# Kernel optimization log

Measured on AMD Instinct MI355X. Metric: run time of the kernel, lower is better.

## Reference

```python
import jax, jax.numpy as jnp
import numpy as np

H = 512     # LSTM_HIDDEN_SIZE
IN = 64     # LSTM_INPUT_SIZE
B = 256
T = 512
OUT = 96    # output_size (decode horizon)


def setup_inputs() -> dict:
    key = jax.random.key(0)
    ks = jax.random.split(key, 32)
    k = 1.0 / np.sqrt(H)
    u = lambda kk, shape: jax.random.uniform(kk, shape, jnp.float32, -k, k)
    inp = {"inputs": jax.random.normal(ks[0], (B, T, IN), jnp.float32)}
    shapes = {
        "enc_Wih0": (4 * H, IN), "enc_Whh0": (4 * H, H), "enc_bih0": (4 * H,), "enc_bhh0": (4 * H,),
        "enc_Wih1": (4 * H, H),  "enc_Whh1": (4 * H, H), "enc_bih1": (4 * H,), "enc_bhh1": (4 * H,),
        "dec_Wih0": (4 * H, 1),  "dec_Whh0": (4 * H, H), "dec_bih0": (4 * H,), "dec_bhh0": (4 * H,),
        "dec_Wih1": (4 * H, H),  "dec_Whh1": (4 * H, H), "dec_bih1": (4 * H,), "dec_bhh1": (4 * H,),
        "proj_W": (1, H), "proj_b": (1,),
    }
    for i, (name, sh) in enumerate(shapes.items()):
        inp[name] = u(ks[i + 1], sh)
    inp["output_size"] = OUT
    return inp


def lstm_cell(x, h, c, Wih, Whh, bih, bhh):
    # PyTorch gate order: i, f, g, o
    z = x @ Wih.T + h @ Whh.T + (bih + bhh)
    i, f, g, o = jnp.split(z, 4, axis=-1)
    c_new = jax.nn.sigmoid(f) * c + jax.nn.sigmoid(i) * jnp.tanh(g)
    h_new = jax.nn.sigmoid(o) * jnp.tanh(c_new)
    return h_new, c_new


def reference(inputs,
              enc_Wih0, enc_Whh0, enc_bih0, enc_bhh0,
              enc_Wih1, enc_Whh1, enc_bih1, enc_bhh1,
              dec_Wih0, dec_Whh0, dec_bih0, dec_bhh0,
              dec_Wih1, dec_Whh1, dec_bih1, dec_bhh1,
              proj_W, proj_b, output_size):
    bsz = inputs.shape[0]
    hdim = enc_Whh0.shape[1]
    z = jnp.zeros((bsz, hdim), inputs.dtype)

    # ---- encoder: 2-layer LSTM over time (batch_first -> time-major scan) ----
    def enc_step(carry, x_t):
        h0, c0, h1, c1 = carry
        h0, c0 = lstm_cell(x_t, h0, c0, enc_Wih0, enc_Whh0, enc_bih0, enc_bhh0)
        h1, c1 = lstm_cell(h0, h1, c1, enc_Wih1, enc_Whh1, enc_bih1, enc_bhh1)
        return (h0, c0, h1, c1), None

    xs = jnp.swapaxes(inputs, 0, 1)  # [T, B, IN]
    (h0, c0, h1, c1), _ = jax.lax.scan(enc_step, (z, z, z, z), xs)

    def dec_step(carry, _):
        h0, c0, h1, c1, x = carry  # x: [B, 1]
        h0, c0 = lstm_cell(x, h0, c0, dec_Wih0, dec_Whh0, dec_bih0, dec_bhh0)
        h1, c1 = lstm_cell(h0, h1, c1, dec_Wih1, dec_Whh1, dec_bih1, dec_bhh1)
        y = h1 @ proj_W.T + proj_b  # [B, 1]
        return (h0, c0, h1, c1, y), y

    x0 = jnp.zeros((bsz, 1), inputs.dtype)
    _, ys = jax.lax.scan(dec_step, (h0, c0, h1, c1, x0), None, length=output_size)
    # ys: [OUT, B, 1] -> [B, OUT, 1]
    return jnp.swapaxes(ys, 0, 1)
```

## Files before the change

### kernel.cpp

```cpp
#include <hip/hip_runtime.h>
#include <math.h>

#define Bb   256
#define Tt   512
#define INn  64
#define Hh   512
#define OUTn 96
#define NWG  256
#define TPB  512
#define SP   (Hh*Bb)
#define RSTRIDE 36
#define HDR  8192

struct Params {
  const float *Xt;
  float *H0, *H1;
  unsigned int *flags;
  unsigned int *rel;
  const float *Wih0,*Whh0,*bih0,*bhh0,*Wih1,*Whh1,*bih1,*bhh1;
  const float *dWih0,*dWhh0,*dbih0,*dbhh0,*dWih1,*dWhh1,*dbih1,*dbhh1;
  const float *projW,*projb;
  float *out;
};

__device__ __forceinline__ float sigm(float x){ return 1.0f/(1.0f + expf(-x)); }

__device__ __forceinline__ void gridbar(unsigned int* flags, unsigned int* rel,
                                        unsigned int g) {
  __syncthreads();
  const int tid = threadIdx.x;
  if (blockIdx.x == 0) {
    if (tid > 0 && tid < NWG) {
      while (__hip_atomic_load(&flags[tid*16], __ATOMIC_RELAXED, __HIP_MEMORY_SCOPE_AGENT) < g)
        __builtin_amdgcn_s_sleep(1);
    }
    __syncthreads();
    if (tid == 0) {
      __threadfence();
      __hip_atomic_store(rel, g, __ATOMIC_RELEASE, __HIP_MEMORY_SCOPE_AGENT);
    }
    __syncthreads();
  } else {
    if (tid == 0) {
      __threadfence();
      __hip_atomic_store(&flags[blockIdx.x*16], g, __ATOMIC_RELEASE, __HIP_MEMORY_SCOPE_AGENT);
      while (__hip_atomic_load(rel, __ATOMIC_RELAXED, __HIP_MEMORY_SCOPE_AGENT) < g)
        __builtin_amdgcn_s_sleep(1);
      __threadfence();
    }
    __syncthreads();
  }
}

__global__ void __launch_bounds__(256) xpose(const float* __restrict__ X, float* __restrict__ Xt) {
  __shared__ float tile[64][65];
  const int t = blockIdx.x;
  const int l = threadIdx.x & 63;
  const int r = threadIdx.x >> 6;
  for (int qd = 0; qd < 4; ++qd) {
    #pragma unroll
    for (int rep = 0; rep < 16; ++rep) {
      int bl = rep*4 + r;
      tile[bl][l] = X[(size_t)(qd*64 + bl)*(Tt*INn) + (size_t)t*INn + l];
    }
    __syncthreads();
    #pragma unroll
    for (int rep = 0; rep < 16; ++rep) {
      int i = rep*4 + r;
      Xt[(size_t)t*(INn*Bb) + (size_t)i*Bb + qd*64 + l] = tile[l][i];
    }
    __syncthreads();
  }
}

__global__ void __launch_bounds__(TPB, 2) lstm_main(Params P) {
  __shared__ float WA[512][16];
  __shared__ float WB[512][8];
  __shared__ float WX[64][8];
  __shared__ float BS[16];
  __shared__ float PW[Hh];
  __shared__ float WXD[8];
  __shared__ float PBs;
  __shared__ float RED[3][128][RSTRIDE];

  const int tid = threadIdx.x;
  const int w   = blockIdx.x;
  const int bq  = tid & 63;
  const int h   = (tid >> 6) & 1;
  const int kh  = tid >> 7;
  const int j   = 2*w + h;
  const int h8  = h*8, h4 = h*4;
  const int slot = h*64 + bq;
  const int b4  = 4*bq;
  unsigned int bg = 1;

  for (int e = tid; e < 512*16; e += TPB) {
    int k = e >> 4, c = e & 15, hh = c >> 3, s = c & 7;
    int unit = 2*w + hh;
    WA[k][c] = (s < 4) ? P.Wih1[(size_t)(s*Hh + unit)*Hh + k]
                       : P.Whh0[(size_t)((s-4)*Hh + unit)*Hh + k];
  }
  for (int e = tid; e < 512*8; e += TPB) {
    int k = e >> 3, c = e & 7, hh = c >> 2, g = c & 3;
    WB[k][c] = P.Whh1[(size_t)(g*Hh + 2*w + hh)*Hh + k];
  }
  for (int e = tid; e < 64*8; e += TPB) {
    int k = e >> 3, c = e & 7, hh = c >> 2, g = c & 3;
    WX[k][c] = P.Wih0[(size_t)(g*Hh + 2*w + hh)*INn + k];
  }
  if (tid < 16) {
    int c = tid, hh = c >> 3, s = c & 7;
    int unit = 2*w + hh;
    BS[c] = (s < 4) ? (P.bih1[s*Hh+unit] + P.bhh1[s*Hh+unit])
                    : (P.bih0[(s-4)*Hh+unit] + P.bhh0[(s-4)*Hh+unit]);
  }
  __syncthreads();

  float c0[4] = {0,0,0,0}, c1[4] = {0,0,0,0};

  for (int p = -1; p <= 511; ++p) {
    float z1i[4], z1f[4], z1g[4], z1o[4];
    float z0i[4], z0f[4], z0g[4], z0o[4];
    #pragma unroll
    for (int m = 0; m < 4; ++m) {
      z1i[m] = (kh==0) ? BS[h8+0] : 0.f; z1f[m] = (kh==0) ? BS[h8+1] : 0.f;
      z1g[m] = (kh==0) ? BS[h8+2] : 0.f; z1o[m] = (kh==0) ? BS[h8+3] : 0.f;
      z0i[m] = (kh==0) ? BS[h8+4] : 0.f; z0f[m] = (kh==0) ? BS[h8+5] : 0.f;
      z0g[m] = (kh==0) ? BS[h8+6] : 0.f; z0o[m] = (kh==0) ? BS[h8+7] : 0.f;
    }
    const float* __restrict__ h0in = P.H0 + (size_t)(p & 1)*SP + b4;
    const float* __restrict__ h1in = P.H1 + (size_t)((p+1) & 1)*SP + b4;
    const int kb = kh*128, ke = kb + 128;
    #pragma unroll 4
    for (int k = kb; k < ke; ++k) {
      const float4 w1 = *reinterpret_cast<const float4*>(&WA[k][h8]);
      const float4 w0 = *reinterpret_cast<const float4*>(&WA[k][h8+4]);
      const float4 wb = *reinterpret_cast<const float4*>(&WB[k][h4]);
      const float4 hv4 = *reinterpret_cast<const float4*>(&h0in[k*Bb]);
      const float4 gv4 = *reinterpret_cast<const float4*>(&h1in[k*Bb]);
      const float* hv = &hv4.x;
      const float* gv = &gv4.x;
      #pragma unroll
      for (int m = 0; m < 4; ++m) {
        z1i[m]=fmaf(w1.x,hv[m],z1i[m]); z1f[m]=fmaf(w1.y,hv[m],z1f[m]);
        z1g[m]=fmaf(w1.z,hv[m],z1g[m]); z1o[m]=fmaf(w1.w,hv[m],z1o[m]);
        z0i[m]=fmaf(w0.x,hv[m],z0i[m]); z0f[m]=fmaf(w0.y,hv[m],z0f[m]);
        z0g[m]=fmaf(w0.z,hv[m],z0g[m]); z0o[m]=fmaf(w0.w,hv[m],z0o[m]);
        z1i[m]=fmaf(wb.x,gv[m],z1i[m]); z1f[m]=fmaf(wb.y,gv[m],z1f[m]);
        z1g[m]=fmaf(wb.z,gv[m],z1g[m]); z1o[m]=fmaf(wb.w,gv[m],z1o[m]);
      }
    }
    {
      int tx = (p+1 < Tt) ? (p+1) : (Tt-1);
      const float* __restrict__ xin = P.Xt + (size_t)tx*(INn*Bb) + b4;
      #pragma unroll 4
      for (int k = kh*16; k < kh*16 + 16; ++k) {
        const float4 wv = *reinterpret_cast<const float4*>(&WX[k][h4]);
        const float4 xv4 = *reinterpret_cast<const float4*>(&xin[k*Bb]);
        const float* xv = &xv4.x;
        #pragma unroll
        for (int m = 0; m < 4; ++m) {
          z0i[m]=fmaf(wv.x,xv[m],z0i[m]); z0f[m]=fmaf(wv.y,xv[m],z0f[m]);
          z0g[m]=fmaf(wv.z,xv[m],z0g[m]); z0o[m]=fmaf(wv.w,xv[m],z0o[m]);
        }
      }
    }
    if (kh) {
      float* r = &RED[kh-1][slot][0];
      *reinterpret_cast<float4*>(&r[ 0]) = make_float4(z1i[0],z1i[1],z1i[2],z1i[3]);
      *reinterpret_cast<float4*>(&r[ 4]) = make_float4(z1f[0],z1f[1],z1f[2],z1f[3]);
      *reinterpret_cast<float4*>(&r[ 8]) = make_float4(z1g[0],z1g[1],z1g[2],z1g[3]);
      *reinterpret_cast<float4*>(&r[12]) = make_float4(z1o[0],z1o[1],z1o[2],z1o[3]);
      *reinterpret_cast<float4*>(&r[16]) = make_float4(z0i[0],z0i[1],z0i[2],z0i[3]);
      *reinterpret_cast<float4*>(&r[20]) = make_float4(z0f[0],z0f[1],z0f[2],z0f[3]);
      *reinterpret_cast<float4*>(&r[24]) = make_float4(z0g[0],z0g[1],z0g[2],z0g[3]);
      *reinterpret_cast<float4*>(&r[28]) = make_float4(z0o[0],z0o[1],z0o[2],z0o[3]);
    }
    __syncthreads();
    if (kh == 0) {
      #pragma unroll
      for (int t = 0; t < 3; ++t) {
        const float* r = &RED[t][slot][0];
        #pragma unroll
        for (int m = 0; m < 4; ++m) {
          z1i[m]+=r[ 0+m]; z1f[m]+=r[ 4+m]; z1g[m]+=r[ 8+m]; z1o[m]+=r[12+m];
          z0i[m]+=r[16+m]; z0f[m]+=r[20+m]; z0g[m]+=r[24+m]; z0o[m]+=r[28+m];
        }
      }
      if (p >= 0) {
        float* st = P.H1 + (size_t)(p & 1)*SP + (size_t)j*Bb + b4;
        float4 o; float* ov = &o.x;
        #pragma unroll
        for (int m = 0; m < 4; ++m) {
          c1[m] = sigm(z1f[m])*c1[m] + sigm(z1i[m])*tanhf(z1g[m]);
          ov[m] = sigm(z1o[m])*tanhf(c1[m]);
        }
        *reinterpret_cast<float4*>(st) = o;
      }
      if (p < 511) {
        float* st = P.H0 + (size_t)((p+1) & 1)*SP + (size_t)j*Bb + b4;
        float4 o; float* ov = &o.x;
        #pragma unroll
        for (int m = 0; m < 4; ++m) {
          c0[m] = sigm(z0f[m])*c0[m] + sigm(z0i[m])*tanhf(z0g[m]);
          ov[m] = sigm(z0o[m])*tanhf(c0[m]);
        }
        *reinterpret_cast<float4*>(st) = o;
      }
    }
    gridbar(P.flags, P.rel, bg); ++bg;
  }

  for (int e = tid; e < 512*16; e += TPB) {
    int k = e >> 4, c = e & 15, hh = c >> 3, s = c & 7;
    int unit = 2*w + hh;
    WA[k][c] = (s < 4) ? P.dWih1[(size_t)(s*Hh + unit)*Hh + k]
                       : P.dWhh1[(size_t)((s-4)*Hh + unit)*Hh + k];
  }
  for (int e = tid; e < 512*8; e += TPB) {
    int k = e >> 3, c = e & 7, hh = c >> 2, g = c & 3;
    WB[k][c] = P.dWhh0[(size_t)(g*Hh + 2*w + hh)*Hh + k];
  }
  if (tid < 8) {
    int c = tid, hh = c >> 2, g = c & 3;
    WXD[c] = P.dWih0[g*Hh + 2*w + hh];
  }
  if (tid >= 16 && tid < 32) {
    int c = tid - 16, hh = c >> 3, s = c & 7;
    int unit = 2*w + hh;
    BS[c] = (s < 4) ? (P.dbih1[s*Hh+unit] + P.dbhh1[s*Hh+unit])
                    : (P.dbih0[(s-4)*Hh+unit] + P.dbhh0[(s-4)*Hh+unit]);
  }
  for (int k = tid; k < Hh; k += TPB) PW[k] = P.projW[k];
  if (tid == 0) PBs = P.projb[0];
  __syncthreads();

  for (int q = 0; q < OUTn; ++q) {
    float xq[4] = {0,0,0,0};
    if (kh == 0 && q > 0) {
      const float* __restrict__ h1p = P.H1 + (size_t)((q+1)&1)*SP + b4;
      float acc[4] = {PBs, PBs, PBs, PBs};
      #pragma unroll 4
      for (int k = 0; k < Hh; ++k) {
        float pw = PW[k];
        const float4 hp4 = *reinterpret_cast<const float4*>(&h1p[k*Bb]);
        const float* hp = &hp4.x;
        #pragma unroll
        for (int m = 0; m < 4; ++m) acc[m] = fmaf(pw, hp[m], acc[m]);
      }
      #pragma unroll
      for (int m = 0; m < 4; ++m) xq[m] = acc[m];
      if (w == 0 && h == 0) {
        #pragma unroll
        for (int m = 0; m < 4; ++m) P.out[(size_t)(b4 + m)*OUTn + (q-1)] = xq[m];
      }
    }
    float zi[4], zf[4], zg[4], zo[4];
    #pragma unroll
    for (int m = 0; m < 4; ++m) {
      zi[m] = (kh==0) ? fmaf(WXD[h4+0], xq[m], BS[h8+4]) : 0.f;
      zf[m] = (kh==0) ? fmaf(WXD[h4+1], xq[m], BS[h8+5]) : 0.f;
      zg[m] = (kh==0) ? fmaf(WXD[h4+2], xq[m], BS[h8+6]) : 0.f;
      zo[m] = (kh==0) ? fmaf(WXD[h4+3], xq[m], BS[h8+7]) : 0.f;
    }
    {
      const float* __restrict__ h0p = P.H0 + (size_t)((q+1)&1)*SP + b4;
      const int kb = kh*128, ke = kb + 128;
      #pragma unroll 4
      for (int k = kb; k < ke; ++k) {
        const float4 wv = *reinterpret_cast<const float4*>(&WB[k][h4]);
        const float4 hv4 = *reinterpret_cast<const float4*>(&h0p[k*Bb]);
        const float* hv = &hv4.x;
        #pragma unroll
        for (int m = 0; m < 4; ++m) {
          zi[m]=fmaf(wv.x,hv[m],zi[m]); zf[m]=fmaf(wv.y,hv[m],zf[m]);
          zg[m]=fmaf(wv.z,hv[m],zg[m]); zo[m]=fmaf(wv.w,hv[m],zo[m]);
        }
      }
    }
    if (kh) {
      float* r = &RED[kh-1][slot][0];
      *reinterpret_cast<float4*>(&r[ 0]) = make_float4(zi[0],zi[1],zi[2],zi[3]);
      *reinterpret_cast<float4*>(&r[ 4]) = make_float4(zf[0],zf[1],zf[2],zf[3]);
      *reinterpret_cast<float4*>(&r[ 8]) = make_float4(zg[0],zg[1],zg[2],zg[3]);
      *reinterpret_cast<float4*>(&r[12]) = make_float4(zo[0],zo[1],zo[2],zo[3]);
    }
    __syncthreads();
    if (kh == 0) {
      #pragma unroll
      for (int t = 0; t < 3; ++t) {
        const float* r = &RED[t][slot][0];
        #pragma unroll
        for (int m = 0; m < 4; ++m) { zi[m]+=r[m]; zf[m]+=r[4+m]; zg[m]+=r[8+m]; zo[m]+=r[12+m]; }
      }
      float* st = P.H0 + (size_t)(q&1)*SP + (size_t)j*Bb + b4;
      float4 o; float* ov = &o.x;
      #pragma unroll
      for (int m = 0; m < 4; ++m) {
        c0[m] = sigm(zf[m])*c0[m] + sigm(zi[m])*tanhf(zg[m]);
        ov[m] = sigm(zo[m])*tanhf(c0[m]);
      }
      *reinterpret_cast<float4*>(st) = o;
    }
    gridbar(P.flags, P.rel, bg); ++bg;

    float yi[4], yf[4], yg[4], yo[4];
    #pragma unroll
    for (int m = 0; m < 4; ++m) {
      yi[m] = (kh==0) ? BS[h8+0] : 0.f; yf[m] = (kh==0) ? BS[h8+1] : 0.f;
      yg[m] = (kh==0) ? BS[h8+2] : 0.f; yo[m] = (kh==0) ? BS[h8+3] : 0.f;
    }
    {
      const float* __restrict__ h0c = P.H0 + (size_t)(q&1)*SP + b4;
      const float* __restrict__ h1q = P.H1 + (size_t)((q+1)&1)*SP + b4;
      const int kb = kh*128, ke = kb + 128;
      #pragma unroll 4
      for (int k = kb; k < ke; ++k) {
        const float4 w1 = *reinterpret_cast<const float4*>(&WA[k][h8]);
        const float4 w2 = *reinterpret_cast<const float4*>(&WA[k][h8+4]);
        const float4 av4 = *reinterpret_cast<const float4*>(&h0c[k*Bb]);
        const float4 dv4 = *reinterpret_cast<const float4*>(&h1q[k*Bb]);
        const float* av = &av4.x;
        const float* dv = &dv4.x;
        #pragma unroll
        for (int m = 0; m < 4; ++m) {
          yi[m]=fmaf(w1.x,av[m],yi[m]); yf[m]=fmaf(w1.y,av[m],yf[m]);
          yg[m]=fmaf(w1.z,av[m],yg[m]); yo[m]=fmaf(w1.w,av[m],yo[m]);
          yi[m]=fmaf(w2.x,dv[m],yi[m]); yf[m]=fmaf(w2.y,dv[m],yf[m]);
          yg[m]=fmaf(w2.z,dv[m],yg[m]); yo[m]=fmaf(w2.w,dv[m],yo[m]);
        }
      }
    }
    if (kh) {
      float* r = &RED[kh-1][slot][0];
      *reinterpret_cast<float4*>(&r[ 0]) = make_float4(yi[0],yi[1],yi[2],yi[3]);
      *reinterpret_cast<float4*>(&r[ 4]) = make_float4(yf[0],yf[1],yf[2],yf[3]);
      *reinterpret_cast<float4*>(&r[ 8]) = make_float4(yg[0],yg[1],yg[2],yg[3]);
      *reinterpret_cast<float4*>(&r[12]) = make_float4(yo[0],yo[1],yo[2],yo[3]);
    }
    __syncthreads();
    if (kh == 0) {
      #pragma unroll
      for (int t = 0; t < 3; ++t) {
        const float* r = &RED[t][slot][0];
        #pragma unroll
        for (int m = 0; m < 4; ++m) { yi[m]+=r[m]; yf[m]+=r[4+m]; yg[m]+=r[8+m]; yo[m]+=r[12+m]; }
      }
      float* st = P.H1 + (size_t)(q&1)*SP + (size_t)j*Bb + b4;
      float4 o; float* ov = &o.x;
      #pragma unroll
      for (int m = 0; m < 4; ++m) {
        c1[m] = sigm(yf[m])*c1[m] + sigm(yi[m])*tanhf(yg[m]);
        ov[m] = sigm(yo[m])*tanhf(c1[m]);
      }
      *reinterpret_cast<float4*>(st) = o;
    }
    gridbar(P.flags, P.rel, bg); ++bg;
  }

  if (kh == 0 && w == 0 && h == 0) {
    const float* __restrict__ h1f = P.H1 + (size_t)((OUTn-1)&1)*SP + b4;
    float acc[4] = {PBs, PBs, PBs, PBs};
    #pragma unroll 4
    for (int k = 0; k < Hh; ++k) {
      float pw = PW[k];
      const float4 hp4 = *reinterpret_cast<const float4*>(&h1f[k*Bb]);
      const float* hp = &hp4.x;
      #pragma unroll
      for (int m = 0; m < 4; ++m) acc[m] = fmaf(pw, hp[m], acc[m]);
    }
    #pragma unroll
    for (int m = 0; m < 4; ++m) P.out[(size_t)(b4 + m)*OUTn + (OUTn-1)] = acc[m];
  }
}

extern "C" void kernel_launch(void* const* d_in, const int* in_sizes, int n_in,
                              void* d_out, int out_size, void* d_ws, size_t ws_size,
                              hipStream_t stream) {
  Params P;
  const float* X = (const float*)d_in[0];
  P.Wih0  = (const float*)d_in[1];  P.Whh0  = (const float*)d_in[2];
  P.bih0  = (const float*)d_in[3];  P.bhh0  = (const float*)d_in[4];
  P.Wih1  = (const float*)d_in[5];  P.Whh1  = (const float*)d_in[6];
  P.bih1  = (const float*)d_in[7];  P.bhh1  = (const float*)d_in[8];
  P.dWih0 = (const float*)d_in[9];  P.dWhh0 = (const float*)d_in[10];
  P.dbih0 = (const float*)d_in[11]; P.dbhh0 = (const float*)d_in[12];
  P.dWih1 = (const float*)d_in[13]; P.dWhh1 = (const float*)d_in[14];
  P.dbih1 = (const float*)d_in[15]; P.dbhh1 = (const float*)d_in[16];
  P.projW = (const float*)d_in[17]; P.projb = (const float*)d_in[18];

  float* ws = (float*)d_ws;
  P.flags = (unsigned int*)ws;
  P.rel   = (unsigned int*)ws + 4096;
  P.H0  = ws + HDR;
  P.H1  = ws + HDR + 2*SP;
  float* Xt = ws + HDR + 4*SP;
  P.Xt  = Xt;
  P.out = (float*)d_out;

  hipMemsetAsync(d_ws, 0, (size_t)(HDR + 4*SP)*sizeof(float), stream);
  hipLaunchKernelGGL(xpose, dim3(Tt), dim3(256), 0, stream, X, Xt);

  void* args[] = { &P };
  hipLaunchCooperativeKernel((void*)lstm_main, dim3(NWG), dim3(TPB), args, 0, stream);
}
```

Before: 28.42 ms.

## Double threads per block and split K-reduction across eight groups with tree reduce

Raises the block size from 512 to 1024 threads so each workgroup splits the hidden-dimension dot products into eight K-slices of 64 instead of four of 128. The cross-slice reduction becomes a two-stage tree through a larger shared buffer, with an extra barrier per phase. The aim is to shorten the serial FMA chain per thread on each recurrent step and hide more global-load latency. In exchange it adds shared-memory traffic and a block-wide sync per phase, drops the two-blocks-per-CU launch hint, and can raise register pressure at the larger block size.

```diff
diff --git a/kernel.cpp b/kernel.cpp
--- a/kernel.cpp
+++ b/kernel.cpp
@@ -7,7 +7,7 @@
 #define Hh   512
 #define OUTn 96
 #define NWG  256
-#define TPB  512
+#define TPB  1024
 #define SP   (Hh*Bb)
 #define RSTRIDE 36
 #define HDR  8192
@@ -73,7 +73,7 @@
   }
 }
 
-__global__ void __launch_bounds__(TPB, 2) lstm_main(Params P) {
+__global__ void __launch_bounds__(TPB) lstm_main(Params P) {
   __shared__ float WA[512][16];
   __shared__ float WB[512][8];
   __shared__ float WX[64][8];
@@ -81,7 +81,7 @@
   __shared__ float PW[Hh];
   __shared__ float WXD[8];
   __shared__ float PBs;
-  __shared__ float RED[3][128][RSTRIDE];
+  __shared__ float RED[4][128][RSTRIDE];
 
   const int tid = threadIdx.x;
   const int w   = blockIdx.x;
@@ -119,18 +119,16 @@
   float c0[4] = {0,0,0,0}, c1[4] = {0,0,0,0};
 
   for (int p = -1; p <= 511; ++p) {
-    float z1i[4], z1f[4], z1g[4], z1o[4];
-    float z0i[4], z0f[4], z0g[4], z0o[4];
-    #pragma unroll
-    for (int m = 0; m < 4; ++m) {
-      z1i[m] = (kh==0) ? BS[h8+0] : 0.f; z1f[m] = (kh==0) ? BS[h8+1] : 0.f;
-      z1g[m] = (kh==0) ? BS[h8+2] : 0.f; z1o[m] = (kh==0) ? BS[h8+3] : 0.f;
-      z0i[m] = (kh==0) ? BS[h8+4] : 0.f; z0f[m] = (kh==0) ? BS[h8+5] : 0.f;
-      z0g[m] = (kh==0) ? BS[h8+6] : 0.f; z0o[m] = (kh==0) ? BS[h8+7] : 0.f;
-    }
+    float z[8][4];
+    #pragma unroll
+    for (int g = 0; g < 8; ++g)
+      #pragma unroll
+      for (int m = 0; m < 4; ++m)
+        z[g][m] = (kh==0) ? BS[h8+g] : 0.f;
+
     const float* __restrict__ h0in = P.H0 + (size_t)(p & 1)*SP + b4;
     const float* __restrict__ h1in = P.H1 + (size_t)((p+1) & 1)*SP + b4;
-    const int kb = kh*128, ke = kb + 128;
+    const int kb = kh*64, ke = kb + 64;
     #pragma unroll 4
     for (int k = kb; k < ke; ++k) {
       const float4 w1 = *reinterpret_cast<const float4*>(&WA[k][h8]);
@@ -142,58 +140,66 @@
       const float* gv = &gv4.x;
       #pragma unroll
       for (int m = 0; m < 4; ++m) {
-        z1i[m]=fmaf(w1.x,hv[m],z1i[m]); z1f[m]=fmaf(w1.y,hv[m],z1f[m]);
-        z1g[m]=fmaf(w1.z,hv[m],z1g[m]); z1o[m]=fmaf(w1.w,hv[m],z1o[m]);
-        z0i[m]=fmaf(w0.x,hv[m],z0i[m]); z0f[m]=fmaf(w0.y,hv[m],z0f[m]);
-        z0g[m]=fmaf(w0.z,hv[m],z0g[m]); z0o[m]=fmaf(w0.w,hv[m],z0o[m]);
-        z1i[m]=fmaf(wb.x,gv[m],z1i[m]); z1f[m]=fmaf(wb.y,gv[m],z1f[m]);
-        z1g[m]=fmaf(wb.z,gv[m],z1g[m]); z1o[m]=fmaf(wb.w,gv[m],z1o[m]);
+        z[0][m]=fmaf(w1.x,hv[m],z[0][m]); z[1][m]=fmaf(w1.y,hv[m],z[1][m]);
+        z[2][m]=fmaf(w1.z,hv[m],z[2][m]); z[3][m]=fmaf(w1.w,hv[m],z[3][m]);
+        z[4][m]=fmaf(w0.x,hv[m],z[4][m]); z[5][m]=fmaf(w0.y,hv[m],z[5][m]);
+        z[6][m]=fmaf(w0.z,hv[m],z[6][m]); z[7][m]=fmaf(w0.w,hv[m],z[7][m]);
+        z[0][m]=fmaf(wb.x,gv[m],z[0][m]); z[1][m]=fmaf(wb.y,gv[m],z[1][m]);
+        z[2][m]=fmaf(wb.z,gv[m],z[2][m]); z[3][m]=fmaf(wb.w,gv[m],z[3][m]);
       }
     }
     {
       int tx = (p+1 < Tt) ? (p+1) : (Tt-1);
       const float* __restrict__ xin = P.Xt + (size_t)tx*(INn*Bb) + b4;
-      #pragma unroll 4
-      for (int k = kh*16; k < kh*16 + 16; ++k) {
+      #pragma unroll
+      for (int k = kh*8; k < kh*8 + 8; ++k) {
         const float4 wv = *reinterpret_cast<const float4*>(&WX[k][h4]);
         const float4 xv4 = *reinterpret_cast<const float4*>(&xin[k*Bb]);
         const float* xv = &xv4.x;
         #pragma unroll
         for (int m = 0; m < 4; ++m) {
-          z0i[m]=fmaf(wv.x,xv[m],z0i[m]); z0f[m]=fmaf(wv.y,xv[m],z0f[m]);
-          z0g[m]=fmaf(wv.z,xv[m],z0g[m]); z0o[m]=fmaf(wv.w,xv[m],z0o[m]);
+          z[4][m]=fmaf(wv.x,xv[m],z[4][m]); z[5][m]=fmaf(wv.y,xv[m],z[5][m]);
+          z[6][m]=fmaf(wv.z,xv[m],z[6][m]); z[7][m]=fmaf(wv.w,xv[m],z[7][m]);
         }
       }
     }
-    if (kh) {
-      float* r = &RED[kh-1][slot][0];
-      *reinterpret_cast<float4*>(&r[ 0]) = make_float4(z1i[0],z1i[1],z1i[2],z1i[3]);
-      *reinterpret_cast<float4*>(&r[ 4]) = make_float4(z1f[0],z1f[1],z1f[2],z1f[3]);
-      *reinterpret_cast<float4*>(&r[ 8]) = make_float4(z1g[0],z1g[1],z1g[2],z1g[3]);
-      *reinterpret_cast<float4*>(&r[12]) = make_float4(z1o[0],z1o[1],z1o[2],z1o[3]);
-      *reinterpret_cast<float4*>(&r[16]) = make_float4(z0i[0],z0i[1],z0i[2],z0i[3]);
-      *reinterpret_cast<float4*>(&r[20]) = make_float4(z0f[0],z0f[1],z0f[2],z0f[3]);
-      *reinterpret_cast<float4*>(&r[24]) = make_float4(z0g[0],z0g[1],z0g[2],z0g[3]);
-      *reinterpret_cast<float4*>(&r[28]) = make_float4(z0o[0],z0o[1],z0o[2],z0o[3]);
+    if (kh >= 4) {
+      float* r = &RED[kh-4][slot][0];
+      #pragma unroll
+      for (int g = 0; g < 8; ++g)
+        *reinterpret_cast<float4*>(&r[g*4]) = make_float4(z[g][0],z[g][1],z[g][2],z[g][3]);
+    }
+    __syncthreads();
+    if (kh < 4) {
+      float* r = &RED[kh][slot][0];
+      #pragma unroll
+      for (int g = 0; g < 8; ++g) {
+        const float4 v = *reinterpret_cast<const float4*>(&r[g*4]);
+        z[g][0]+=v.x; z[g][1]+=v.y; z[g][2]+=v.z; z[g][3]+=v.w;
+      }
+      if (kh > 0) {
+        #pragma unroll
+        for (int g = 0; g < 8; ++g)
+          *reinterpret_cast<float4*>(&r[g*4]) = make_float4(z[g][0],z[g][1],z[g][2],z[g][3]);
+      }
     }
     __syncthreads();
     if (kh == 0) {
       #pragma unroll
-      for (int t = 0; t < 3; ++t) {
+      for (int t = 1; t < 4; ++t) {
         const float* r = &RED[t][slot][0];
         #pragma unroll
-        for (int m = 0; m < 4; ++m) {
-          z1i[m]+=r[ 0+m]; z1f[m]+=r[ 4+m]; z1g[m]+=r[ 8+m]; z1o[m]+=r[12+m];
-          z0i[m]+=r[16+m]; z0f[m]+=r[20+m]; z0g[m]+=r[24+m]; z0o[m]+=r[28+m];
-        }
+        for (int g = 0; g < 8; ++g)
+          #pragma unroll
+          for (int m = 0; m < 4; ++m) z[g][m] += r[g*4+m];
       }
       if (p >= 0) {
         float* st = P.H1 + (size_t)(p & 1)*SP + (size_t)j*Bb + b4;
         float4 o; float* ov = &o.x;
         #pragma unroll
         for (int m = 0; m < 4; ++m) {
-          c1[m] = sigm(z1f[m])*c1[m] + sigm(z1i[m])*tanhf(z1g[m]);
-          ov[m] = sigm(z1o[m])*tanhf(c1[m]);
+          c1[m] = sigm(z[1][m])*c1[m] + sigm(z[0][m])*tanhf(z[2][m]);
+          ov[m] = sigm(z[3][m])*tanhf(c1[m]);
         }
         *reinterpret_cast<float4*>(st) = o;
       }
@@ -202,8 +208,8 @@
         float4 o; float* ov = &o.x;
         #pragma unroll
         for (int m = 0; m < 4; ++m) {
-          c0[m] = sigm(z0f[m])*c0[m] + sigm(z0i[m])*tanhf(z0g[m]);
-          ov[m] = sigm(z0o[m])*tanhf(c0[m]);
+          c0[m] = sigm(z[5][m])*c0[m] + sigm(z[4][m])*tanhf(z[6][m]);
+          ov[m] = sigm(z[7][m])*tanhf(c0[m]);
         }
         *reinterpret_cast<float4*>(st) = o;
       }
@@ -255,17 +261,15 @@
         for (int m = 0; m < 4; ++m) P.out[(size_t)(b4 + m)*OUTn + (q-1)] = xq[m];
       }
     }
-    float zi[4], zf[4], zg[4], zo[4];
-    #pragma unroll
-    for (int m = 0; m < 4; ++m) {
-      zi[m] = (kh==0) ? fmaf(WXD[h4+0], xq[m], BS[h8+4]) : 0.f;
-      zf[m] = (kh==0) ? fmaf(WXD[h4+1], xq[m], BS[h8+5]) : 0.f;
-      zg[m] = (kh==0) ? fmaf(WXD[h4+2], xq[m], BS[h8+6]) : 0.f;
-      zo[m] = (kh==0) ? fmaf(WXD[h4+3], xq[m], BS[h8+7]) : 0.f;
-    }
+    float zd[4][4];
+    #pragma unroll
+    for (int g = 0; g < 4; ++g)
+      #pragma unroll
+      for (int m = 0; m < 4; ++m)
+        zd[g][m] = (kh==0) ? fmaf(WXD[h4+g], xq[m], BS[h8+4+g]) : 0.f;
     {
       const float* __restrict__ h0p = P.H0 + (size_t)((q+1)&1)*SP + b4;
-      const int kb = kh*128, ke = kb + 128;
+      const int kb = kh*64, ke = kb + 64;
       #pragma unroll 4
       for (int k = kb; k < ke; ++k) {
         const float4 wv = *reinterpret_cast<const float4*>(&WB[k][h4]);
@@ -273,47 +277,62 @@
         const float* hv = &hv4.x;
         #pragma unroll
         for (int m = 0; m < 4; ++m) {
-          zi[m]=fmaf(wv.x,hv[m],zi[m]); zf[m]=fmaf(wv.y,hv[m],zf[m]);
-          zg[m]=fmaf(wv.z,hv[m],zg[m]); zo[m]=fmaf(wv.w,hv[m],zo[m]);
+          zd[0][m]=fmaf(wv.x,hv[m],zd[0][m]); zd[1][m]=fmaf(wv.y,hv[m],zd[1][m]);
+          zd[2][m]=fmaf(wv.z,hv[m],zd[2][m]); zd[3][m]=fmaf(wv.w,hv[m],zd[3][m]);
         }
       }
     }
-    if (kh) {
-      float* r = &RED[kh-1][slot][0];
-      *reinterpret_cast<float4*>(&r[ 0]) = make_float4(zi[0],zi[1],zi[2],zi[3]);
-      *reinterpret_cast<float4*>(&r[ 4]) = make_float4(zf[0],zf[1],zf[2],zf[3]);
-      *reinterpret_cast<float4*>(&r[ 8]) = make_float4(zg[0],zg[1],zg[2],zg[3]);
-      *reinterpret_cast<float4*>(&r[12]) = make_float4(zo[0],zo[1],zo[2],zo[3]);
+    if (kh >= 4) {
+      float* r = &RED[kh-4][slot][0];
+      #pragma unroll
+      for (int g = 0; g < 4; ++g)
+        *reinterpret_cast<float4*>(&r[g*4]) = make_float4(zd[g][0],zd[g][1],zd[g][2],zd[g][3]);
+    }
+    __syncthreads();
+    if (kh < 4) {
+      float* r = &RED[kh][slot][0];
+      #pragma unroll
+      for (int g = 0; g < 4; ++g) {
+        const float4 v = *reinterpret_cast<const float4*>(&r[g*4]);
+        zd[g][0]+=v.x; zd[g][1]+=v.y; zd[g][2]+=v.z; zd[g][3]+=v.w;
+      }
+      if (kh > 0) {
+        #pragma unroll
+        for (int g = 0; g < 4; ++g)
+          *reinterpret_cast<float4*>(&r[g*4]) = make_float4(zd[g][0],zd[g][1],zd[g][2],zd[g][3]);
+      }
     }
     __syncthreads();
     if (kh == 0) {
       #pragma unroll
-      for (int t = 0; t < 3; ++t) {
+      for (int t = 1; t < 4; ++t) {
         const float* r = &RED[t][slot][0];
         #pragma unroll
-        for (int m = 0; m < 4; ++m) { zi[m]+=r[m]; zf[m]+=r[4+m]; zg[m]+=r[8+m]; zo[m]+=r[12+m]; }
+        for (int g = 0; g < 4; ++g)
+          #pragma unroll
+          for (int m = 0; m < 4; ++m) zd[g][m] += r[g*4+m];
       }
       float* st = P.H0 + (size_t)(q&1)*SP + (size_t)j*Bb + b4;
       float4 o; float* ov = &o.x;
       #pragma unroll
       for (int m = 0; m < 4; ++m) {
-        c0[m] = sigm(zf[m])*c0[m] + sigm(zi[m])*tanhf(zg[m]);
-        ov[m] = sigm(zo[m])*tanhf(c0[m]);
+        c0[m] = sigm(zd[1][m])*c0[m] + sigm(zd[0][m])*tanhf(zd[2][m]);
+        ov[m] = sigm(zd[3][m])*tanhf(c0[m]);
       }
       *reinterpret_cast<float4*>(st) = o;
     }
     gridbar(P.flags, P.rel, bg); ++bg;
 
-    float yi[4], yf[4], yg[4], yo[4];
-    #pragma unroll
-    for (int m = 0; m < 4; ++m) {
-      yi[m] = (kh==0) ? BS[h8+0] : 0.f; yf[m] = (kh==0) ? BS[h8+1] : 0.f;
-      yg[m] = (kh==0) ? BS[h8+2] : 0.f; yo[m] = (kh==0) ? BS[h8+3] : 0.f;
-    }
+    float y[4][4];
+    #pragma unroll
+    for (int g = 0; g < 4; ++g)
+      #pragma unroll
+      for (int m = 0; m < 4; ++m)
+        y[g][m] = (kh==0) ? BS[h8+g] : 0.f;
     {
       const float* __restrict__ h0c = P.H0 + (size_t)(q&1)*SP + b4;
       const float* __restrict__ h1q = P.H1 + (size_t)((q+1)&1)*SP + b4;
-      const int kb = kh*128, ke = kb + 128;
+      const int kb = kh*64, ke = kb + 64;
       #pragma unroll 4
       for (int k = kb; k < ke; ++k) {
         const float4 w1 = *reinterpret_cast<const float4*>(&WA[k][h8]);
@@ -324,34 +343,49 @@
         const float* dv = &dv4.x;
         #pragma unroll
         for (int m = 0; m < 4; ++m) {
-          yi[m]=fmaf(w1.x,av[m],yi[m]); yf[m]=fmaf(w1.y,av[m],yf[m]);
-          yg[m]=fmaf(w1.z,av[m],yg[m]); yo[m]=fmaf(w1.w,av[m],yo[m]);
-          yi[m]=fmaf(w2.x,dv[m],yi[m]); yf[m]=fmaf(w2.y,dv[m],yf[m]);
-          yg[m]=fmaf(w2.z,dv[m],yg[m]); yo[m]=fmaf(w2.w,dv[m],yo[m]);
+          y[0][m]=fmaf(w1.x,av[m],y[0][m]); y[1][m]=fmaf(w1.y,av[m],y[1][m]);
+          y[2][m]=fmaf(w1.z,av[m],y[2][m]); y[3][m]=fmaf(w1.w,av[m],y[3][m]);
+          y[0][m]=fmaf(w2.x,dv[m],y[0][m]); y[1][m]=fmaf(w2.y,dv[m],y[1][m]);
+          y[2][m]=fmaf(w2.z,dv[m],y[2][m]); y[3][m]=fmaf(w2.w,dv[m],y[3][m]);
         }
       }
     }
-    if (kh) {
-      float* r = &RED[kh-1][slot][0];
-      *reinterpret_cast<float4*>(&r[ 0]) = make_float4(yi[0],yi[1],yi[2],yi[3]);
-      *reinterpret_cast<float4*>(&r[ 4]) = make_float4(yf[0],yf[1],yf[2],yf[3]);
-      *reinterpret_cast<float4*>(&r[ 8]) = make_float4(yg[0],yg[1],yg[2],yg[3]);
-      *reinterpret_cast<float4*>(&r[12]) = make_float4(yo[0],yo[1],yo[2],yo[3]);
+    if (kh >= 4) {
+      float* r = &RED[kh-4][slot][0];
+      #pragma unroll
+      for (int g = 0; g < 4; ++g)
+        *reinterpret_cast<float4*>(&r[g*4]) = make_float4(y[g][0],y[g][1],y[g][2],y[g][3]);
+    }
+    __syncthreads();
+    if (kh < 4) {
+      float* r = &RED[kh][slot][0];
+      #pragma unroll
+      for (int g = 0; g < 4; ++g) {
+        const float4 v = *reinterpret_cast<const float4*>(&r[g*4]);
+        y[g][0]+=v.x; y[g][1]+=v.y; y[g][2]+=v.z; y[g][3]+=v.w;
+      }
+      if (kh > 0) {
+        #pragma unroll
+        for (int g = 0; g < 4; ++g)
+          *reinterpret_cast<float4*>(&r[g*4]) = make_float4(y[g][0],y[g][1],y[g][2],y[g][3]);
+      }
     }
     __syncthreads();
     if (kh == 0) {
       #pragma unroll
-      for (int t = 0; t < 3; ++t) {
+      for (int t = 1; t < 4; ++t) {
         const float* r = &RED[t][slot][0];
         #pragma unroll
-        for (int m = 0; m < 4; ++m) { yi[m]+=r[m]; yf[m]+=r[4+m]; yg[m]+=r[8+m]; yo[m]+=r[12+m]; }
+        for (int g = 0; g < 4; ++g)
+          #pragma unroll
+          for (int m = 0; m < 4; ++m) y[g][m] += r[g*4+m];
       }
       float* st = P.H1 + (size_t)(q&1)*SP + (size_t)j*Bb + b4;
       float4 o; float* ov = &o.x;
       #pragma unroll
       for (int m = 0; m < 4; ++m) {
-        c1[m] = sigm(yf[m])*c1[m] + sigm(yi[m])*tanhf(yg[m]);
-        ov[m] = sigm(yo[m])*tanhf(c1[m]);
+        c1[m] = sigm(y[1][m])*c1[m] + sigm(y[0][m])*tanhf(y[2][m]);
+        ov[m] = sigm(y[3][m])*tanhf(c1[m]);
       }
       *reinterpret_cast<float4*>(st) = o;
     }
```

Measured after the change: 32.96 ms. 16.0% more time.

## Double block threads and split gate computation across two thread groups

Applied to the files above, without the earlier changes.

The block grows from 512 to 1024 threads. A new gate-half index makes each thread accumulate two of the four gates per layer instead of all four, which halves its FMA chain and register footprint. The gate nonlinearities are exchanged through a new shared buffer and an extra __syncthreads. In the decoder, the projection dot product is now split across the k-quarters and reduced through shared memory, so it is no longer computed serially by the kh==0 threads. The cost is an extra block barrier per step, twice as many loads of the h vectors, and lower occupancy per CU.

```diff
diff --git a/kernel.cpp b/kernel.cpp
--- a/kernel.cpp
+++ b/kernel.cpp
@@ -7,9 +7,9 @@
 #define Hh   512
 #define OUTn 96
 #define NWG  256
-#define TPB  512
+#define TPB  1024
 #define SP   (Hh*Bb)
-#define RSTRIDE 36
+#define RST  20
 #define HDR  8192
 
 struct Params {
@@ -73,7 +73,7 @@
   }
 }
 
-__global__ void __launch_bounds__(TPB, 2) lstm_main(Params P) {
+__global__ void __launch_bounds__(TPB) lstm_main(Params P) {
   __shared__ float WA[512][16];
   __shared__ float WB[512][8];
   __shared__ float WX[64][8];
@@ -81,15 +81,17 @@
   __shared__ float PW[Hh];
   __shared__ float WXD[8];
   __shared__ float PBs;
-  __shared__ float RED[3][128][RSTRIDE];
+  __shared__ float RED[3][2][128][RST];
+  __shared__ float XRED[128][RST];
 
   const int tid = threadIdx.x;
   const int w   = blockIdx.x;
   const int bq  = tid & 63;
   const int h   = (tid >> 6) & 1;
-  const int kh  = tid >> 7;
+  const int gh  = (tid >> 7) & 1;
+  const int kh  = tid >> 8;
   const int j   = 2*w + h;
-  const int h8  = h*8, h4 = h*4;
+  const int h8  = h*8, h4 = h*4, g2 = gh*2;
   const int slot = h*64 + bq;
   const int b4  = 4*bq;
   unsigned int bg = 1;
@@ -119,81 +121,85 @@
   float c0[4] = {0,0,0,0}, c1[4] = {0,0,0,0};
 
   for (int p = -1; p <= 511; ++p) {
-    float z1i[4], z1f[4], z1g[4], z1o[4];
-    float z0i[4], z0f[4], z0g[4], z0o[4];
+    float zA[4], zB[4], zC[4], zD[4];
     #pragma unroll
     for (int m = 0; m < 4; ++m) {
-      z1i[m] = (kh==0) ? BS[h8+0] : 0.f; z1f[m] = (kh==0) ? BS[h8+1] : 0.f;
-      z1g[m] = (kh==0) ? BS[h8+2] : 0.f; z1o[m] = (kh==0) ? BS[h8+3] : 0.f;
-      z0i[m] = (kh==0) ? BS[h8+4] : 0.f; z0f[m] = (kh==0) ? BS[h8+5] : 0.f;
-      z0g[m] = (kh==0) ? BS[h8+6] : 0.f; z0o[m] = (kh==0) ? BS[h8+7] : 0.f;
+      zA[m] = (kh==0) ? BS[h8+g2]   : 0.f;
+      zB[m] = (kh==0) ? BS[h8+g2+1] : 0.f;
+      zC[m] = (kh==0) ? BS[h8+4+g2] : 0.f;
+      zD[m] = (kh==0) ? BS[h8+5+g2] : 0.f;
     }
     const float* __restrict__ h0in = P.H0 + (size_t)(p & 1)*SP + b4;
     const float* __restrict__ h1in = P.H1 + (size_t)((p+1) & 1)*SP + b4;
     const int kb = kh*128, ke = kb + 128;
     #pragma unroll 4
     for (int k = kb; k < ke; ++k) {
-      const float4 w1 = *reinterpret_cast<const float4*>(&WA[k][h8]);
-      const float4 w0 = *reinterpret_cast<const float4*>(&WA[k][h8+4]);
-      const float4 wb = *reinterpret_cast<const float4*>(&WB[k][h4]);
+      const float2 w1 = *reinterpret_cast<const float2*>(&WA[k][h8+g2]);
+      const float2 w0 = *reinterpret_cast<const float2*>(&WA[k][h8+4+g2]);
+      const float2 wb = *reinterpret_cast<const float2*>(&WB[k][h4+g2]);
       const float4 hv4 = *reinterpret_cast<const float4*>(&h0in[k*Bb]);
       const float4 gv4 = *reinterpret_cast<const float4*>(&h1in[k*Bb]);
       const float* hv = &hv4.x;
       const float* gv = &gv4.x;
       #pragma unroll
       for (int m = 0; m < 4; ++m) {
-        z1i[m]=fmaf(w1.x,hv[m],z1i[m]); z1f[m]=fmaf(w1.y,hv[m],z1f[m]);
-        z1g[m]=fmaf(w1.z,hv[m],z1g[m]); z1o[m]=fmaf(w1.w,hv[m],z1o[m]);
-        z0i[m]=fmaf(w0.x,hv[m],z0i[m]); z0f[m]=fmaf(w0.y,hv[m],z0f[m]);
-        z0g[m]=fmaf(w0.z,hv[m],z0g[m]); z0o[m]=fmaf(w0.w,hv[m],z0o[m]);
-        z1i[m]=fmaf(wb.x,gv[m],z1i[m]); z1f[m]=fmaf(wb.y,gv[m],z1f[m]);
-        z1g[m]=fmaf(wb.z,gv[m],z1g[m]); z1o[m]=fmaf(wb.w,gv[m],z1o[m]);
+        zA[m]=fmaf(w1.x,hv[m],zA[m]); zB[m]=fmaf(w1.y,hv[m],zB[m]);
+        zA[m]=fmaf(wb.x,gv[m],zA[m]); zB[m]=fmaf(wb.y,gv[m],zB[m]);
+        zC[m]=fmaf(w0.x,hv[m],zC[m]); zD[m]=fmaf(w0.y,hv[m],zD[m]);
       }
     }
     {
       int tx = (p+1 < Tt) ? (p+1) : (Tt-1);
       const float* __restrict__ xin = P.Xt + (size_t)tx*(INn*Bb) + b4;
-      #pragma unroll 4
+      #pragma unroll
       for (int k = kh*16; k < kh*16 + 16; ++k) {
-        const float4 wv = *reinterpret_cast<const float4*>(&WX[k][h4]);
+        const float2 wx = *reinterpret_cast<const float2*>(&WX[k][h4+g2]);
         const float4 xv4 = *reinterpret_cast<const float4*>(&xin[k*Bb]);
         const float* xv = &xv4.x;
         #pragma unroll
         for (int m = 0; m < 4; ++m) {
-          z0i[m]=fmaf(wv.x,xv[m],z0i[m]); z0f[m]=fmaf(wv.y,xv[m],z0f[m]);
-          z0g[m]=fmaf(wv.z,xv[m],z0g[m]); z0o[m]=fmaf(wv.w,xv[m],z0o[m]);
+          zC[m]=fmaf(wx.x,xv[m],zC[m]); zD[m]=fmaf(wx.y,xv[m],zD[m]);
         }
       }
     }
     if (kh) {
-      float* r = &RED[kh-1][slot][0];
-      *reinterpret_cast<float4*>(&r[ 0]) = make_float4(z1i[0],z1i[1],z1i[2],z1i[3]);
-      *reinterpret_cast<float4*>(&r[ 4]) = make_float4(z1f[0],z1f[1],z1f[2],z1f[3]);
-      *reinterpret_cast<float4*>(&r[ 8]) = make_float4(z1g[0],z1g[1],z1g[2],z1g[3]);
-      *reinterpret_cast<float4*>(&r[12]) = make_float4(z1o[0],z1o[1],z1o[2],z1o[3]);
-      *reinterpret_cast<float4*>(&r[16]) = make_float4(z0i[0],z0i[1],z0i[2],z0i[3]);
-      *reinterpret_cast<float4*>(&r[20]) = make_float4(z0f[0],z0f[1],z0f[2],z0f[3]);
-      *reinterpret_cast<float4*>(&r[24]) = make_float4(z0g[0],z0g[1],z0g[2],z0g[3]);
-      *reinterpret_cast<float4*>(&r[28]) = make_float4(z0o[0],z0o[1],z0o[2],z0o[3]);
+      float* r = &RED[kh-1][gh][slot][0];
+      *reinterpret_cast<float4*>(&r[ 0]) = make_float4(zA[0],zA[1],zA[2],zA[3]);
+      *reinterpret_cast<float4*>(&r[ 4]) = make_float4(zB[0],zB[1],zB[2],zB[3]);
+      *reinterpret_cast<float4*>(&r[ 8]) = make_float4(zC[0],zC[1],zC[2],zC[3]);
+      *reinterpret_cast<float4*>(&r[12]) = make_float4(zD[0],zD[1],zD[2],zD[3]);
     }
     __syncthreads();
     if (kh == 0) {
       #pragma unroll
       for (int t = 0; t < 3; ++t) {
-        const float* r = &RED[t][slot][0];
-        #pragma unroll
-        for (int m = 0; m < 4; ++m) {
-          z1i[m]+=r[ 0+m]; z1f[m]+=r[ 4+m]; z1g[m]+=r[ 8+m]; z1o[m]+=r[12+m];
-          z0i[m]+=r[16+m]; z0f[m]+=r[20+m]; z0g[m]+=r[24+m]; z0o[m]+=r[28+m];
-        }
-      }
+        const float* r = &RED[t][gh][slot][0];
+        #pragma unroll
+        for (int m = 0; m < 4; ++m) {
+          zA[m]+=r[m]; zB[m]+=r[4+m]; zC[m]+=r[8+m]; zD[m]+=r[12+m];
+        }
+      }
+      if (gh == 1) {
+        float* x = &XRED[slot][0];
+        #pragma unroll
+        for (int m = 0; m < 4; ++m) {
+          x[m]    = tanhf(zA[m]);
+          x[4+m]  = sigm(zB[m]);
+          x[8+m]  = tanhf(zC[m]);
+          x[12+m] = sigm(zD[m]);
+        }
+      }
+    }
+    __syncthreads();
+    if (kh == 0 && gh == 0) {
+      const float* x = &XRED[slot][0];
       if (p >= 0) {
         float* st = P.H1 + (size_t)(p & 1)*SP + (size_t)j*Bb + b4;
         float4 o; float* ov = &o.x;
         #pragma unroll
         for (int m = 0; m < 4; ++m) {
-          c1[m] = sigm(z1f[m])*c1[m] + sigm(z1i[m])*tanhf(z1g[m]);
-          ov[m] = sigm(z1o[m])*tanhf(c1[m]);
+          c1[m] = sigm(zB[m])*c1[m] + sigm(zA[m])*x[m];
+          ov[m] = x[4+m]*tanhf(c1[m]);
         }
         *reinterpret_cast<float4*>(st) = o;
       }
@@ -202,8 +208,8 @@
         float4 o; float* ov = &o.x;
         #pragma unroll
         for (int m = 0; m < 4; ++m) {
-          c0[m] = sigm(z0f[m])*c0[m] + sigm(z0i[m])*tanhf(z0g[m]);
-          ov[m] = sigm(z0o[m])*tanhf(c0[m]);
+          c0[m] = sigm(zD[m])*c0[m] + sigm(zC[m])*x[8+m];
+          ov[m] = x[12+m]*tanhf(c0[m]);
         }
         *reinterpret_cast<float4*>(st) = o;
       }
@@ -237,78 +243,87 @@
 
   for (int q = 0; q < OUTn; ++q) {
     float xq[4] = {0,0,0,0};
-    if (kh == 0 && q > 0) {
+    if (q > 0) {
       const float* __restrict__ h1p = P.H1 + (size_t)((q+1)&1)*SP + b4;
-      float acc[4] = {PBs, PBs, PBs, PBs};
+      if (kh == 0) { xq[0]=PBs; xq[1]=PBs; xq[2]=PBs; xq[3]=PBs; }
+      const int kb = kh*128, ke = kb + 128;
       #pragma unroll 4
-      for (int k = 0; k < Hh; ++k) {
+      for (int k = kb; k < ke; ++k) {
         float pw = PW[k];
         const float4 hp4 = *reinterpret_cast<const float4*>(&h1p[k*Bb]);
         const float* hp = &hp4.x;
         #pragma unroll
-        for (int m = 0; m < 4; ++m) acc[m] = fmaf(pw, hp[m], acc[m]);
-      }
-      #pragma unroll
-      for (int m = 0; m < 4; ++m) xq[m] = acc[m];
-      if (w == 0 && h == 0) {
-        #pragma unroll
-        for (int m = 0; m < 4; ++m) P.out[(size_t)(b4 + m)*OUTn + (q-1)] = xq[m];
-      }
-    }
-    float zi[4], zf[4], zg[4], zo[4];
+        for (int m = 0; m < 4; ++m) xq[m] = fmaf(pw, hp[m], xq[m]);
+      }
+    }
+    float zC[4], zD[4];
     #pragma unroll
     for (int m = 0; m < 4; ++m) {
-      zi[m] = (kh==0) ? fmaf(WXD[h4+0], xq[m], BS[h8+4]) : 0.f;
-      zf[m] = (kh==0) ? fmaf(WXD[h4+1], xq[m], BS[h8+5]) : 0.f;
-      zg[m] = (kh==0) ? fmaf(WXD[h4+2], xq[m], BS[h8+6]) : 0.f;
-      zo[m] = (kh==0) ? fmaf(WXD[h4+3], xq[m], BS[h8+7]) : 0.f;
+      zC[m] = (kh==0) ? BS[h8+4+g2] : 0.f;
+      zD[m] = (kh==0) ? BS[h8+5+g2] : 0.f;
     }
     {
       const float* __restrict__ h0p = P.H0 + (size_t)((q+1)&1)*SP + b4;
       const int kb = kh*128, ke = kb + 128;
       #pragma unroll 4
       for (int k = kb; k < ke; ++k) {
-        const float4 wv = *reinterpret_cast<const float4*>(&WB[k][h4]);
+        const float2 wv = *reinterpret_cast<const float2*>(&WB[k][h4+g2]);
         const float4 hv4 = *reinterpret_cast<const float4*>(&h0p[k*Bb]);
         const float* hv = &hv4.x;
         #pragma unroll
         for (int m = 0; m < 4; ++m) {
-          zi[m]=fmaf(wv.x,hv[m],zi[m]); zf[m]=fmaf(wv.y,hv[m],zf[m]);
-          zg[m]=fmaf(wv.z,hv[m],zg[m]); zo[m]=fmaf(wv.w,hv[m],zo[m]);
+          zC[m]=fmaf(wv.x,hv[m],zC[m]); zD[m]=fmaf(wv.y,hv[m],zD[m]);
         }
       }
     }
     if (kh) {
-      float* r = &RED[kh-1][slot][0];
-      *reinterpret_cast<float4*>(&r[ 0]) = make_float4(zi[0],zi[1],zi[2],zi[3]);
-      *reinterpret_cast<float4*>(&r[ 4]) = make_float4(zf[0],zf[1],zf[2],zf[3]);
-      *reinterpret_cast<float4*>(&r[ 8]) = make_float4(zg[0],zg[1],zg[2],zg[3]);
-      *reinterpret_cast<float4*>(&r[12]) = make_float4(zo[0],zo[1],zo[2],zo[3]);
+      float* r = &RED[kh-1][gh][slot][0];
+      *reinterpret_cast<float4*>(&r[ 0]) = make_float4(zC[0],zC[1],zC[2],zC[3]);
+      *reinterpret_cast<float4*>(&r[ 4]) = make_float4(zD[0],zD[1],zD[2],zD[3]);
+      *reinterpret_cast<float4*>(&r[ 8]) = make_float4(xq[0],xq[1],xq[2],xq[3]);
     }
     __syncthreads();
     if (kh == 0) {
       #pragma unroll
       for (int t = 0; t < 3; ++t) {
-        const float* r = &RED[t][slot][0];
-        #pragma unroll
-        for (int m = 0; m < 4; ++m) { zi[m]+=r[m]; zf[m]+=r[4+m]; zg[m]+=r[8+m]; zo[m]+=r[12+m]; }
-      }
+        const float* r = &RED[t][gh][slot][0];
+        #pragma unroll
+        for (int m = 0; m < 4; ++m) { zC[m]+=r[m]; zD[m]+=r[4+m]; xq[m]+=r[8+m]; }
+      }
+      if (gh == 0 && w == 0 && h == 0 && q > 0) {
+        #pragma unroll
+        for (int m = 0; m < 4; ++m) P.out[(size_t)(b4 + m)*OUTn + (q-1)] = xq[m];
+      }
+      #pragma unroll
+      for (int m = 0; m < 4; ++m) {
+        zC[m] = fmaf(WXD[h4+g2],   xq[m], zC[m]);
+        zD[m] = fmaf(WXD[h4+g2+1], xq[m], zD[m]);
+      }
+      if (gh == 1) {
+        float* x = &XRED[slot][0];
+        #pragma unroll
+        for (int m = 0; m < 4; ++m) { x[m] = tanhf(zC[m]); x[4+m] = sigm(zD[m]); }
+      }
+    }
+    __syncthreads();
+    if (kh == 0 && gh == 0) {
+      const float* x = &XRED[slot][0];
       float* st = P.H0 + (size_t)(q&1)*SP + (size_t)j*Bb + b4;
       float4 o; float* ov = &o.x;
       #pragma unroll
       for (int m = 0; m < 4; ++m) {
-        c0[m] = sigm(zf[m])*c0[m] + sigm(zi[m])*tanhf(zg[m]);
-        ov[m] = sigm(zo[m])*tanhf(c0[m]);
+        c0[m] = sigm(zD[m])*c0[m] + sigm(zC[m])*x[m];
+        ov[m] = x[4+m]*tanhf(c0[m]);
       }
       *reinterpret_cast<float4*>(st) = o;
     }
     gridbar(P.flags, P.rel, bg); ++bg;
 
-    float yi[4], yf[4], yg[4], yo[4];
+    float zA[4], zB[4];
     #pragma unroll
     for (int m = 0; m < 4; ++m) {
-      yi[m] = (kh==0) ? BS[h8+0] : 0.f; yf[m] = (kh==0) ? BS[h8+1] : 0.f;
-      yg[m] = (kh==0) ? BS[h8+2] : 0.f; yo[m] = (kh==0) ? BS[h8+3] : 0.f;
+      zA[m] = (kh==0) ? BS[h8+g2]   : 0.f;
+      zB[m] = (kh==0) ? BS[h8+g2+1] : 0.f;
     }
     {
       const float* __restrict__ h0c = P.H0 + (size_t)(q&1)*SP + b4;
@@ -316,49 +331,54 @@
       const int kb = kh*128, ke = kb + 128;
       #pragma unroll 4
       for (int k = kb; k < ke; ++k) {
-        const float4 w1 = *reinterpret_cast<const float4*>(&WA[k][h8]);
-        const float4 w2 = *reinterpret_cast<const float4*>(&WA[k][h8+4]);
+        const float2 w1 = *reinterpret_cast<const float2*>(&WA[k][h8+g2]);
+        const float2 w2 = *reinterpret_cast<const float2*>(&WA[k][h8+4+g2]);
         const float4 av4 = *reinterpret_cast<const float4*>(&h0c[k*Bb]);
         const float4 dv4 = *reinterpret_cast<const float4*>(&h1q[k*Bb]);
         const float* av = &av4.x;
         const float* dv = &dv4.x;
         #pragma unroll
         for (int m = 0; m < 4; ++m) {
-          yi[m]=fmaf(w1.x,av[m],yi[m]); yf[m]=fmaf(w1.y,av[m],yf[m]);
-          yg[m]=fmaf(w1.z,av[m],yg[m]); yo[m]=fmaf(w1.w,av[m],yo[m]);
-          yi[m]=fmaf(w2.x,dv[m],yi[m]); yf[m]=fmaf(w2.y,dv[m],yf[m]);
-          yg[m]=fmaf(w2.z,dv[m],yg[m]); yo[m]=fmaf(w2.w,dv[m],yo[m]);
+          zA[m]=fmaf(w1.x,av[m],zA[m]); zB[m]=fmaf(w1.y,av[m],zB[m]);
+          zA[m]=fmaf(w2.x,dv[m],zA[m]); zB[m]=fmaf(w2.y,dv[m],zB[m]);
         }
       }
     }
     if (kh) {
-      float* r = &RED[kh-1][slot][0];
-      *reinterpret_cast<float4*>(&r[ 0]) = make_float4(yi[0],yi[1],yi[2],yi[3]);
-      *reinterpret_cast<float4*>(&r[ 4]) = make_float4(yf[0],yf[1],yf[2],yf[3]);
-      *reinterpret_cast<float4*>(&r[ 8]) = make_float4(yg[0],yg[1],yg[2],yg[3]);
-      *reinterpret_cast<float4*>(&r[12]) = make_float4(yo[0],yo[1],yo[2],yo[3]);
+      float* r = &RED[kh-1][gh][slot][0];
+      *reinterpret_cast<float4*>(&r[0]) = make_float4(zA[0],zA[1],zA[2],zA[3]);
+      *reinterpret_cast<float4*>(&r[4]) = make_float4(zB[0],zB[1],zB[2],zB[3]);
     }
     __syncthreads();
     if (kh == 0) {
       #pragma unroll
       for (int t = 0; t < 3; ++t) {
-        const float* r = &RED[t][slot][0];
-        #pragma unroll
-        for (int m = 0; m < 4; ++m) { yi[m]+=r[m]; yf[m]+=r[4+m]; yg[m]+=r[8+m]; yo[m]+=r[12+m]; }
-      }
+        const float* r = &RED[t][gh][slot][0];
+        #pragma unroll
+        for (int m = 0; m < 4; ++m) { zA[m]+=r[m]; zB[m]+=r[4+m]; }
+      }
+      if (gh == 1) {
+        float* x = &XRED[slot][0];
+        #pragma unroll
+        for (int m = 0; m < 4; ++m) { x[m] = tanhf(zA[m]); x[4+m] = sigm(zB[m]); }
+      }
+    }
+    __syncthreads();
+    if (kh == 0 && gh == 0) {
+      const float* x = &XRED[slot][0];
       float* st = P.H1 + (size_t)(q&1)*SP + (size_t)j*Bb + b4;
       float4 o; float* ov = &o.x;
       #pragma unroll
       for (int m = 0; m < 4; ++m) {
-        c1[m] = sigm(yf[m])*c1[m] + sigm(yi[m])*tanhf(yg[m]);
-        ov[m] = sigm(yo[m])*tanhf(c1[m]);
+        c1[m] = sigm(zB[m])*c1[m] + sigm(zA[m])*x[m];
+        ov[m] = x[4+m]*tanhf(c1[m]);
       }
       *reinterpret_cast<float4*>(st) = o;
     }
     gridbar(P.flags, P.rel, bg); ++bg;
   }
 
-  if (kh == 0 && w == 0 && h == 0) {
+  if (kh == 0 && gh == 0 && h == 0 && w == 0) {
     const float* __restrict__ h1f = P.H1 + (size_t)((OUTn-1)&1)*SP + b4;
     float acc[4] = {PBs, PBs, PBs, PBs};
     #pragma unroll 4
```

New measurement: 38.86 ms. 36.7% more time.
